# Kernel tuning notes

Hardware: AMD Instinct MI355X
Metric: run time of the kernel (lower is better)

Reference implementation:

```python
import jax, jax.numpy as jnp
import numpy as np
import math

OMEGA_0 = 30.0
LAYER_SIZES = [3, 256, 256, 256, 256, 3]
N_POINTS = 524288


def _siren_params(key):
    """SIREN initialization matching the original module."""
    keys = jax.random.split(key, len(LAYER_SIZES) - 1)
    params = {}
    for i in range(len(LAYER_SIZES) - 1):
        in_dim, out_dim = LAYER_SIZES[i], LAYER_SIZES[i + 1]
        k = keys[i]
        bound = (1.0 / in_dim) if i == 0 else (math.sqrt(6.0 / in_dim) / OMEGA_0)
        W = jax.random.uniform(k, (out_dim, in_dim), minval=-bound, maxval=bound, dtype=jnp.float32)
        b = jax.random.uniform(k, (out_dim,), minval=-1e-6, maxval=1e-6, dtype=jnp.float32)
        params[f"W{i}"] = W
        params[f"b{i}"] = b
    return params


def setup_inputs() -> dict:
    key = jax.random.key(0)
    kx, kp = jax.random.split(key)
    # coordinates in [-1, 1], typical SIREN input domain
    x = jax.random.uniform(kx, (N_POINTS, 3), minval=-1.0, maxval=1.0, dtype=jnp.float32)
    inp = {"x": x}
    inp.update(_siren_params(kp))
    return inp


def reference(x, W0, b0, W1, b1, W2, b2, W3, b3, W4, b4):
    # First layer: sin(omega_0 * (W0 @ x + b0)), batched over rows of x.
    h = jnp.sin(OMEGA_0 * (jnp.einsum("ni,oi->no", x, W0) + b0))
    # Hidden layers: sin(W @ h + b)
    h = jnp.sin(jnp.einsum("ni,oi->no", h, W1) + b1)
    h = jnp.sin(jnp.einsum("ni,oi->no", h, W2) + b2)
    h = jnp.sin(jnp.einsum("ni,oi->no", h, W3) + b3)
    # Final layer: linear, no activation.
    out = jnp.einsum("ni,oi->no", h, W4) + b4
    return out
```

## Files before the change

kernel.cpp:

```cpp
#include <hip/hip_runtime.h>
#include <stdint.h>


typedef float    f32x4 __attribute__((ext_vector_type(4)));
typedef short    s16x8 __attribute__((ext_vector_type(8)));
typedef uint32_t u32x2 __attribute__((ext_vector_type(2)));
typedef uint32_t u32x4 __attribute__((ext_vector_type(4)));

#define INV2PI 0.15915494309189535f
#define L0SCALE 4.774648292756860f
#define W4OFF 196608

__device__ __forceinline__ uint16_t f32_to_bf16(float f) {
    uint32_t u = __builtin_bit_cast(uint32_t, f);
    u += 0x7FFFu + ((u >> 16) & 1u);
    return (uint16_t)(u >> 16);
}
__device__ __forceinline__ uint32_t pack_bf16x2(float lo, float hi) {
#if __has_builtin(__builtin_amdgcn_cvt_pk_bf16_f32)
    auto v = __builtin_amdgcn_cvt_pk_bf16_f32(lo, hi);
    return __builtin_bit_cast(uint32_t, v);
#else
    uint32_t a = __builtin_bit_cast(uint32_t, lo);
    uint32_t b = __builtin_bit_cast(uint32_t, hi);
    a += 0x7FFFu + ((a >> 16) & 1u);
    b += 0x7FFFu + ((b >> 16) & 1u);
    return (a >> 16) | (b & 0xFFFF0000u);
#endif
}
__device__ __forceinline__ float sin_rev(float r) {
    return __builtin_amdgcn_sinf(r);
}

__global__ void convert_weights(const float* __restrict__ W1,
                                const float* __restrict__ W2,
                                const float* __restrict__ W3,
                                const float* __restrict__ W4,
                                uint16_t* __restrict__ wsb) {
    int tid = blockIdx.x * blockDim.x + threadIdx.x;
    if (tid < 196608) {
        int l = tid >> 16;
        int r = tid & 65535;
        int c = r >> 8;
        int k = r & 255;
        const float* W = (l == 0) ? W1 : (l == 1) ? W2 : W3;
        int kc = k >> 5, q = (k >> 3) & 3, j = k & 7;
        wsb[(((l * 8 + kc) * 16 + (c >> 4)) * 64 + q * 16 + (c & 15)) * 8 + j] =
            f32_to_bf16(W[c * 256 + k] * INV2PI);
    } else if (tid < 200704) {
        int e = tid - 196608;
        int kc = e >> 9, lane = (e >> 3) & 63, j = e & 7;
        int n16 = lane & 15, q = lane >> 4;
        float v = (n16 < 3) ? W4[n16 * 256 + kc * 32 + q * 8 + j] : 0.0f;
        wsb[W4OFF + (kc * 64 + lane) * 8 + j] = f32_to_bf16(v);
    }
}

__global__ __launch_bounds__(256, 3) void siren_main(
    const float* __restrict__ x,
    const float* __restrict__ W0, const float* __restrict__ b0,
    const float* __restrict__ b1, const float* __restrict__ b2,
    const float* __restrict__ b3,
    const float* __restrict__ b4,
    const uint16_t* __restrict__ Wb,
    float* __restrict__ out)
{
    __shared__ uint16_t h_lds[2048 * 8];

    const int tid  = threadIdx.x;
    const int lane = tid & 63;
    const int wid  = tid >> 6;
    const int n16  = lane & 15;
    const int q    = lane >> 4;
    const int p0   = blockIdx.x * 64;

    {
        float xv[4][3];
        #pragma unroll
        for (int rt = 0; rt < 4; ++rt) {
            const float* xp = x + (p0 + rt * 16 + n16) * 3;
            xv[rt][0] = xp[0]; xv[rt][1] = xp[1]; xv[rt][2] = xp[2];
        }
        #pragma unroll
        for (int oo = 0; oo < 2; ++oo) {
            const int octet = wid * 8 + oo * 4 + q;
            const float* w0r = W0 + octet * 24;
            float wv[24];
            #pragma unroll
            for (int i = 0; i < 24; ++i) wv[i] = w0r[i] * L0SCALE;
            float bb[8];
            #pragma unroll
            for (int i = 0; i < 8; ++i) bb[i] = b0[octet * 8 + i] * L0SCALE;
            const int kc0 = octet >> 2, q0 = octet & 3;
            #pragma unroll
            for (int rt = 0; rt < 4; ++rt) {
                u32x4 pk;
                #pragma unroll
                for (int j2 = 0; j2 < 4; ++j2) {
                    float za = wv[(2*j2  )*3+0] * xv[rt][0] +
                               wv[(2*j2  )*3+1] * xv[rt][1] +
                               wv[(2*j2  )*3+2] * xv[rt][2] + bb[2*j2];
                    float zb = wv[(2*j2+1)*3+0] * xv[rt][0] +
                               wv[(2*j2+1)*3+1] * xv[rt][1] +
                               wv[(2*j2+1)*3+2] * xv[rt][2] + bb[2*j2+1];
                    pk[j2] = pack_bf16x2(sin_rev(za), sin_rev(zb));
                }
                *(u32x4*)&h_lds[((kc0 * 4 + rt) * 64 + q0 * 16 + n16) * 8] = pk;
            }
        }
    }
    __syncthreads();

    #pragma unroll
    for (int l = 0; l < 3; ++l) {
        const uint16_t* wsl = Wb + l * 65536;
        const float* bl = (l == 0) ? b1 : (l == 1) ? b2 : b3;

        s16x8 Wbuf[2][2][4];
        #pragma unroll
        for (int kc2 = 0; kc2 < 2; ++kc2)
            #pragma unroll
            for (int t = 0; t < 4; ++t)
                Wbuf[0][kc2][t] = *(const s16x8*)(wsl + ((kc2 * 16 + wid * 4 + t) * 64 + lane) * 8);

        f32x4 acc[4][4];
        #pragma unroll
        for (int t = 0; t < 4; ++t) {
            f32x4 bv = *(const f32x4*)&bl[wid * 64 + t * 16 + q * 4];
            bv *= INV2PI;
            #pragma unroll
            for (int pt = 0; pt < 4; ++pt) acc[t][pt] = bv;
        }

        #pragma unroll
        for (int kp = 0; kp < 4; ++kp) {
            const int cur = kp & 1, nxt = cur ^ 1;
            if (kp < 3) {
                #pragma unroll
                for (int kc2 = 0; kc2 < 2; ++kc2)
                    #pragma unroll
                    for (int t = 0; t < 4; ++t)
                        Wbuf[nxt][kc2][t] = *(const s16x8*)(wsl +
                            (((kp * 2 + 2 + kc2) * 16 + wid * 4 + t) * 64 + lane) * 8);
            }
            #pragma unroll
            for (int kc2 = 0; kc2 < 2; ++kc2) {
                const int kc = kp * 2 + kc2;
                s16x8 hf[4];
                #pragma unroll
                for (int pt = 0; pt < 4; ++pt)
                    hf[pt] = *(const s16x8*)&h_lds[((kc * 4 + pt) * 64 + lane) * 8];
                #pragma unroll
                for (int t = 0; t < 4; ++t)
                    #pragma unroll
                    for (int pt = 0; pt < 4; ++pt)
                        acc[t][pt] = __builtin_amdgcn_mfma_f32_16x16x32_bf16(
                            Wbuf[cur][kc2][t], hf[pt], acc[t][pt], 0, 0, 0);
            }
        }
        __syncthreads();

        uint32_t* hw = (uint32_t*)h_lds;
        #pragma unroll
        for (int t = 0; t < 4; ++t) {
            const int kcp = wid * 2 + (t >> 1);
            const int qp  = (t * 2 + (q >> 1)) & 3;
            #pragma unroll
            for (int pt = 0; pt < 4; ++pt) {
                float s0 = sin_rev(acc[t][pt][0]);
                float s1 = sin_rev(acc[t][pt][1]);
                float s2 = sin_rev(acc[t][pt][2]);
                float s3 = sin_rev(acc[t][pt][3]);
                int base = ((kcp * 4 + pt) * 64 + qp * 16 + n16) * 4 + (q & 1) * 2;
                u32x2 w2 = { pack_bf16x2(s0, s1), pack_bf16x2(s2, s3) };
                *(u32x2*)&hw[base] = w2;
            }
        }
        __syncthreads();
    }

    {
        float bb4 = (n16 < 3) ? b4[n16] : 0.0f;
        f32x4 accF = { bb4, bb4, bb4, bb4 };
        #pragma unroll
        for (int kc = 0; kc < 8; ++kc) {
            s16x8 w4f = *(const s16x8*)(Wb + W4OFF + (kc * 64 + lane) * 8);
            s16x8 af  = *(const s16x8*)&h_lds[((kc * 4 + wid) * 64 + lane) * 8];
            accF = __builtin_amdgcn_mfma_f32_16x16x32_bf16(af, w4f, accF, 0, 0, 0);
        }
        if (n16 < 3) {
            #pragma unroll
            for (int r = 0; r < 4; ++r)
                out[(p0 + wid * 16 + q * 4 + r) * 3 + n16] = accF[r];
        }
    }
}

extern "C" void kernel_launch(void* const* d_in, const int* in_sizes, int n_in,
                              void* d_out, int out_size, void* d_ws, size_t ws_size,
                              hipStream_t stream) {
    const float* x  = (const float*)d_in[0];
    const float* W0 = (const float*)d_in[1];
    const float* b0 = (const float*)d_in[2];
    const float* W1 = (const float*)d_in[3];
    const float* b1 = (const float*)d_in[4];
    const float* W2 = (const float*)d_in[5];
    const float* b2 = (const float*)d_in[6];
    const float* W3 = (const float*)d_in[7];
    const float* b3 = (const float*)d_in[8];
    const float* W4 = (const float*)d_in[9];
    const float* b4 = (const float*)d_in[10];
    float* outp     = (float*)d_out;
    uint16_t* wsb   = (uint16_t*)d_ws;

    hipLaunchKernelGGL(convert_weights, dim3(784), dim3(256), 0, stream,
                       W1, W2, W3, W4, wsb);
    hipLaunchKernelGGL(siren_main, dim3(8192), dim3(256), 0, stream,
                       x, W0, b0, b1, b2, b3, b4, wsb, outp);
}
```

Baseline: 300.1 us.

## Prefetch next layer's weights across layer boundaries and use LDS-only barriers

The first bf16 weight chunk of each hidden layer, and the final-layer W4 fragments, are now loaded into the register double buffer during the last K-step of the previous stage. The first chunk is also issued before the layer-0 sine computation. This hides global-load latency at every layer transition. `__syncthreads` is replaced by an inline-asm `s_waitcnt lgkmcnt(0); s_barrier`, which waits only on LDS traffic, so the prefetched global loads can stay in flight across barriers. In exchange, register pressure rises and the hand-written barrier relies on the compiler still inserting the correct vmcnt waits before the weights are used.

```diff
diff --git a/kernel.cpp b/kernel.cpp
--- a/kernel.cpp
+++ b/kernel.cpp
@@ -10,6 +10,8 @@
 #define INV2PI 0.15915494309189535f
 #define L0SCALE 4.774648292756860f
 #define W4OFF 196608
+
+#define SYNC_LDS() asm volatile("s_waitcnt lgkmcnt(0)\n\ts_barrier" ::: "memory")
 
 __device__ __forceinline__ uint16_t f32_to_bf16(float f) {
     uint32_t u = __builtin_bit_cast(uint32_t, f);
@@ -74,6 +76,16 @@
     const int q    = lane >> 4;
     const int p0   = blockIdx.x * 64;
 
+    s16x8 Wbuf[2][2][4];
+
+    #pragma unroll
+    for (int kc2 = 0; kc2 < 2; ++kc2)
+        #pragma unroll
+        for (int t = 0; t < 4; ++t)
+            Wbuf[0][kc2][t] = *(const s16x8*)(Wb + ((kc2 * 16 + wid * 4 + t) * 64 + lane) * 8);
+
+    const float bb4 = (n16 < 3) ? b4[n16] : 0.0f;
+
     {
         float xv[4][3];
         #pragma unroll
@@ -109,20 +121,13 @@
             }
         }
     }
-    __syncthreads();
+    SYNC_LDS();
 
     #pragma unroll
     for (int l = 0; l < 3; ++l) {
         const uint16_t* wsl = Wb + l * 65536;
         const float* bl = (l == 0) ? b1 : (l == 1) ? b2 : b3;
 
-        s16x8 Wbuf[2][2][4];
-        #pragma unroll
-        for (int kc2 = 0; kc2 < 2; ++kc2)
-            #pragma unroll
-            for (int t = 0; t < 4; ++t)
-                Wbuf[0][kc2][t] = *(const s16x8*)(wsl + ((kc2 * 16 + wid * 4 + t) * 64 + lane) * 8);
-
         f32x4 acc[4][4];
         #pragma unroll
         for (int t = 0; t < 4; ++t) {
@@ -142,6 +147,21 @@
                     for (int t = 0; t < 4; ++t)
                         Wbuf[nxt][kc2][t] = *(const s16x8*)(wsl +
                             (((kp * 2 + 2 + kc2) * 16 + wid * 4 + t) * 64 + lane) * 8);
+            } else if (l < 2) {
+                const uint16_t* wsn = Wb + (l + 1) * 65536;
+                #pragma unroll
+                for (int kc2 = 0; kc2 < 2; ++kc2)
+                    #pragma unroll
+                    for (int t = 0; t < 4; ++t)
+                        Wbuf[nxt][kc2][t] = *(const s16x8*)(wsn +
+                            ((kc2 * 16 + wid * 4 + t) * 64 + lane) * 8);
+            } else {
+                #pragma unroll
+                for (int kc2 = 0; kc2 < 2; ++kc2)
+                    #pragma unroll
+                    for (int t = 0; t < 4; ++t)
+                        Wbuf[nxt][kc2][t] = *(const s16x8*)(Wb + W4OFF +
+                            (((kc2 * 4 + t) * 64 + lane) * 8));
             }
             #pragma unroll
             for (int kc2 = 0; kc2 < 2; ++kc2) {
@@ -158,7 +178,7 @@
                             Wbuf[cur][kc2][t], hf[pt], acc[t][pt], 0, 0, 0);
             }
         }
-        __syncthreads();
+        SYNC_LDS();
 
         uint32_t* hw = (uint32_t*)h_lds;
         #pragma unroll
@@ -176,17 +196,16 @@
                 *(u32x2*)&hw[base] = w2;
             }
         }
-        __syncthreads();
+        SYNC_LDS();
     }
 
     {
-        float bb4 = (n16 < 3) ? b4[n16] : 0.0f;
         f32x4 accF = { bb4, bb4, bb4, bb4 };
         #pragma unroll
         for (int kc = 0; kc < 8; ++kc) {
-            s16x8 w4f = *(const s16x8*)(Wb + W4OFF + (kc * 64 + lane) * 8);
-            s16x8 af  = *(const s16x8*)&h_lds[((kc * 4 + wid) * 64 + lane) * 8];
-            accF = __builtin_amdgcn_mfma_f32_16x16x32_bf16(af, w4f, accF, 0, 0, 0);
+            s16x8 af = *(const s16x8*)&h_lds[((kc * 4 + wid) * 64 + lane) * 8];
+            accF = __builtin_amdgcn_mfma_f32_16x16x32_bf16(
+                af, Wbuf[0][kc >> 2][kc & 3], accF, 0, 0, 0);
         }
         if (n16 < 3) {
             #pragma unroll
```

Measured after the change: 307.0 us. 1.02x slower.

## Switch hidden layers to 32x32x16 bf16 MFMA with new weight and LDS layouts

Applied to the files above, without the earlier changes.

Replaces the 16x16x32 MFMA tiling of the hidden layers with 32x32x16 MFMA instructions. Each wave now computes a 64x64 output tile as 2x2 blocks of 32x32. The weight pre-conversion layout, the LDS activation layout, the bias broadcast and the final-layer LDS read indexing are all reworked to match. The goal is fewer MFMA issues and fewer LDS fragment loads per FLOP, at the cost of a riskier layout remap that must stay correct across all layers.

```diff
diff --git a/kernel.cpp b/kernel.cpp
--- a/kernel.cpp
+++ b/kernel.cpp
@@ -2,10 +2,11 @@
 #include <stdint.h>
 
 
-typedef float    f32x4 __attribute__((ext_vector_type(4)));
-typedef short    s16x8 __attribute__((ext_vector_type(8)));
-typedef uint32_t u32x2 __attribute__((ext_vector_type(2)));
-typedef uint32_t u32x4 __attribute__((ext_vector_type(4)));
+typedef float    f32x4  __attribute__((ext_vector_type(4)));
+typedef float    f32x16 __attribute__((ext_vector_type(16)));
+typedef short    s16x8  __attribute__((ext_vector_type(8)));
+typedef uint32_t u32x2  __attribute__((ext_vector_type(2)));
+typedef uint32_t u32x4  __attribute__((ext_vector_type(4)));
 
 #define INV2PI 0.15915494309189535f
 #define L0SCALE 4.774648292756860f
@@ -44,8 +45,8 @@
         int c = r >> 8;
         int k = r & 255;
         const float* W = (l == 0) ? W1 : (l == 1) ? W2 : W3;
-        int kc = k >> 5, q = (k >> 3) & 3, j = k & 7;
-        wsb[(((l * 8 + kc) * 16 + (c >> 4)) * 64 + q * 16 + (c & 15)) * 8 + j] =
+        int s = k >> 4, h = (k >> 3) & 1, j = k & 7, g = c >> 5;
+        wsb[(((l * 16 + s) * 8 + g) * 64 + h * 32 + (c & 31)) * 8 + j] =
             f32_to_bf16(W[c * 256 + k] * INV2PI);
     } else if (tid < 200704) {
         int e = tid - 196608;
@@ -72,6 +73,8 @@
     const int wid  = tid >> 6;
     const int n16  = lane & 15;
     const int q    = lane >> 4;
+    const int la   = lane & 31;
+    const int h5   = lane >> 5;
     const int p0   = blockIdx.x * 64;
 
     {
@@ -91,7 +94,6 @@
             float bb[8];
             #pragma unroll
             for (int i = 0; i < 8; ++i) bb[i] = b0[octet * 8 + i] * L0SCALE;
-            const int kc0 = octet >> 2, q0 = octet & 3;
             #pragma unroll
             for (int rt = 0; rt < 4; ++rt) {
                 u32x4 pk;
@@ -105,7 +107,7 @@
                                wv[(2*j2+1)*3+2] * xv[rt][2] + bb[2*j2+1];
                     pk[j2] = pack_bf16x2(sin_rev(za), sin_rev(zb));
                 }
-                *(u32x4*)&h_lds[((kc0 * 4 + rt) * 64 + q0 * 16 + n16) * 8] = pk;
+                *(u32x4*)&h_lds[(octet * 64 + rt * 16 + n16) * 8] = pk;
             }
         }
     }
@@ -118,18 +120,25 @@
 
         s16x8 Wbuf[2][2][4];
         #pragma unroll
-        for (int kc2 = 0; kc2 < 2; ++kc2)
-            #pragma unroll
-            for (int t = 0; t < 4; ++t)
-                Wbuf[0][kc2][t] = *(const s16x8*)(wsl + ((kc2 * 16 + wid * 4 + t) * 64 + lane) * 8);
-
-        f32x4 acc[4][4];
-        #pragma unroll
-        for (int t = 0; t < 4; ++t) {
-            f32x4 bv = *(const f32x4*)&bl[wid * 64 + t * 16 + q * 4];
-            bv *= INV2PI;
-            #pragma unroll
-            for (int pt = 0; pt < 4; ++pt) acc[t][pt] = bv;
+        for (int ct = 0; ct < 2; ++ct)
+            #pragma unroll
+            for (int i = 0; i < 4; ++i)
+                Wbuf[0][ct][i] = *(const s16x8*)(wsl +
+                    ((i * 8 + wid * 2 + ct) * 64 + lane) * 8);
+
+        f32x16 acc[2][2];
+        #pragma unroll
+        for (int ct = 0; ct < 2; ++ct) {
+            f32x16 bv;
+            #pragma unroll
+            for (int Q = 0; Q < 4; ++Q) {
+                f32x4 b4v = *(const f32x4*)&bl[wid * 64 + ct * 32 + 8 * Q + 4 * h5];
+                b4v *= INV2PI;
+                #pragma unroll
+                for (int m = 0; m < 4; ++m) bv[Q * 4 + m] = b4v[m];
+            }
+            acc[ct][0] = bv;
+            acc[ct][1] = bv;
         }
 
         #pragma unroll
@@ -137,43 +146,45 @@
             const int cur = kp & 1, nxt = cur ^ 1;
             if (kp < 3) {
                 #pragma unroll
-                for (int kc2 = 0; kc2 < 2; ++kc2)
+                for (int ct = 0; ct < 2; ++ct)
                     #pragma unroll
-                    for (int t = 0; t < 4; ++t)
-                        Wbuf[nxt][kc2][t] = *(const s16x8*)(wsl +
-                            (((kp * 2 + 2 + kc2) * 16 + wid * 4 + t) * 64 + lane) * 8);
-            }
-            #pragma unroll
-            for (int kc2 = 0; kc2 < 2; ++kc2) {
-                const int kc = kp * 2 + kc2;
-                s16x8 hf[4];
-                #pragma unroll
-                for (int pt = 0; pt < 4; ++pt)
-                    hf[pt] = *(const s16x8*)&h_lds[((kc * 4 + pt) * 64 + lane) * 8];
-                #pragma unroll
-                for (int t = 0; t < 4; ++t)
+                    for (int i = 0; i < 4; ++i)
+                        Wbuf[nxt][ct][i] = *(const s16x8*)(wsl +
+                            (((kp * 4 + 4 + i) * 8 + wid * 2 + ct) * 64 + lane) * 8);
+            }
+            #pragma unroll
+            for (int i = 0; i < 4; ++i) {
+                const int s = kp * 4 + i;
+                s16x8 hf[2];
+                #pragma unroll
+                for (int pt = 0; pt < 2; ++pt)
+                    hf[pt] = *(const s16x8*)&h_lds[
+                        ((s * 2 + h5) * 64 + pt * 32 + la) * 8];
+                #pragma unroll
+                for (int ct = 0; ct < 2; ++ct)
                     #pragma unroll
-                    for (int pt = 0; pt < 4; ++pt)
-                        acc[t][pt] = __builtin_amdgcn_mfma_f32_16x16x32_bf16(
-                            Wbuf[cur][kc2][t], hf[pt], acc[t][pt], 0, 0, 0);
+                    for (int pt = 0; pt < 2; ++pt)
+                        acc[ct][pt] = __builtin_amdgcn_mfma_f32_32x32x16_bf16(
+                            Wbuf[cur][ct][i], hf[pt], acc[ct][pt], 0, 0, 0);
             }
         }
         __syncthreads();
 
         uint32_t* hw = (uint32_t*)h_lds;
         #pragma unroll
-        for (int t = 0; t < 4; ++t) {
-            const int kcp = wid * 2 + (t >> 1);
-            const int qp  = (t * 2 + (q >> 1)) & 3;
-            #pragma unroll
-            for (int pt = 0; pt < 4; ++pt) {
-                float s0 = sin_rev(acc[t][pt][0]);
-                float s1 = sin_rev(acc[t][pt][1]);
-                float s2 = sin_rev(acc[t][pt][2]);
-                float s3 = sin_rev(acc[t][pt][3]);
-                int base = ((kcp * 4 + pt) * 64 + qp * 16 + n16) * 4 + (q & 1) * 2;
-                u32x2 w2 = { pack_bf16x2(s0, s1), pack_bf16x2(s2, s3) };
-                *(u32x2*)&hw[base] = w2;
+        for (int ct = 0; ct < 2; ++ct) {
+            #pragma unroll
+            for (int Q = 0; Q < 4; ++Q) {
+                #pragma unroll
+                for (int pt = 0; pt < 2; ++pt) {
+                    float s0 = sin_rev(acc[ct][pt][Q * 4 + 0]);
+                    float s1 = sin_rev(acc[ct][pt][Q * 4 + 1]);
+                    float s2 = sin_rev(acc[ct][pt][Q * 4 + 2]);
+                    float s3 = sin_rev(acc[ct][pt][Q * 4 + 3]);
+                    int u = (wid * 8 + ct * 4 + Q) * 64 + pt * 32 + la;
+                    u32x2 w2 = { pack_bf16x2(s0, s1), pack_bf16x2(s2, s3) };
+                    *(u32x2*)&hw[u * 4 + h5 * 2] = w2;
+                }
             }
         }
         __syncthreads();
@@ -185,7 +196,8 @@
         #pragma unroll
         for (int kc = 0; kc < 8; ++kc) {
             s16x8 w4f = *(const s16x8*)(Wb + W4OFF + (kc * 64 + lane) * 8);
-            s16x8 af  = *(const s16x8*)&h_lds[((kc * 4 + wid) * 64 + lane) * 8];
+            s16x8 af  = *(const s16x8*)&h_lds[
+                ((kc * 4 + q) * 64 + wid * 16 + n16) * 8];
             accF = __builtin_amdgcn_mfma_f32_16x16x32_bf16(af, w4f, accF, 0, 0, 0);
         }
         if (n16 < 3) {
```

Result: slower. 322.5 us (+7.5%).
